# Performance work log

Hardware: AMD Instinct MI355X
Metric: run time of the kernel (lower is better)

Reference implementation:

```python
import math
import jax, jax.numpy as jnp
import numpy as np

FACTOR = 5
N_HEADS = 8


def setup_inputs() -> dict:
    key = jax.random.key(0)
    ks = jax.random.split(key, 9)
    B, S, D = 4, 8192, 512
    s = 0.02
    x = jax.random.normal(ks[0], (B, S, D), jnp.float32)
    Wq = jax.random.normal(ks[1], (D, D), jnp.float32) * s
    bq = jax.random.normal(ks[2], (D,), jnp.float32) * s
    Wk = jax.random.normal(ks[3], (D, D), jnp.float32) * s
    bk = jax.random.normal(ks[4], (D,), jnp.float32) * s
    Wv = jax.random.normal(ks[5], (D, D), jnp.float32) * s
    bv = jax.random.normal(ks[6], (D,), jnp.float32) * s
    Wo = jax.random.normal(ks[7], (D, D), jnp.float32) * s
    bo = jax.random.normal(ks[8], (D,), jnp.float32) * s
    return {"x": x, "Wq": Wq, "bq": bq, "Wk": Wk, "bk": bk,
            "Wv": Wv, "bv": bv, "Wo": Wo, "bo": bo}


def reference(x, Wq, bq, Wk, bk, Wv, bv, Wo, bo):
    B, S, D = x.shape
    H = N_HEADS
    hd = D // H
    scale = hd ** -0.5

    def proj(W, b):
        # [B,S,D] -> [B,H,S,hd]
        return (x @ W + b).reshape(B, S, H, hd).transpose(0, 2, 1, 3)

    q = proj(Wq, bq)
    k = proj(Wk, bk)
    v = proj(Wv, bv)

    # number of "active" queries: O(log S)
    sampled = max(1, min(S, int(FACTOR * math.log(S + 1))))

    sparsity = jnp.sum(q * q, axis=-1)                    # [B,H,S]
    top_idx = jax.lax.top_k(sparsity, sampled)[1]         # [B,H,u]

    sel_q = jnp.take_along_axis(q, top_idx[..., None], axis=2)  # [B,H,u,hd]
    scores = jnp.einsum('bhud,bhsd->bhus', sel_q, k) * scale     # [B,H,u,S]
    attn = jax.nn.softmax(scores, axis=-1)
    sel_ctx = jnp.einsum('bhus,bhsd->bhud', attn, v)             # [B,H,u,hd]

    # default context = mean of values; overwrite rows of selected queries
    ctx = jnp.broadcast_to(v.mean(axis=2, keepdims=True), (B, H, S, hd))
    bi = jnp.arange(B)[:, None, None]
    hi = jnp.arange(H)[None, :, None]
    ctx = ctx.at[bi, hi, top_idx].set(sel_ctx)                   # scatter [B,H,S,hd]

    ctx = ctx.transpose(0, 2, 1, 3).reshape(B, S, D)
    return ctx @ Wo + bo
```

## Files before the change

### kernel.cpp

```cpp
#include <hip/hip_runtime.h>
#include <hip/hip_fp16.h>
#include <math.h>

#define B_ 4
#define S_ 8192
#define D_ 512
#define H_ 8
#define U_ 45
#define NCHUNK 16

typedef unsigned short ushortT;
typedef __attribute__((ext_vector_type(8))) _Float16 half8;
typedef __attribute__((ext_vector_type(4))) float f32x4;

__device__ __forceinline__ ushortT f2h(float f) {
    return __half_as_ushort(__float2half(f));
}
__device__ __forceinline__ float h2f(ushortT u) {
    return __half2float(__ushort_as_half(u));
}

__device__ __forceinline__ void gload_lds16(const ushortT* g, ushortT* l) {
    __builtin_amdgcn_global_load_lds(
        (const __attribute__((address_space(1))) void*)g,
        (__attribute__((address_space(3))) void*)l,
        16, 0, 0);
}

__global__ __launch_bounds__(256) void prep_kernel(
    const float* __restrict__ X, ushortT* __restrict__ Xf,
    const float* __restrict__ Wq, const float* __restrict__ Wk,
    const float* __restrict__ Wv,
    ushortT* __restrict__ WqT, ushortT* __restrict__ WkT,
    ushortT* __restrict__ WvT,
    float* __restrict__ vsum, float* __restrict__ outbase)
{
    __shared__ float t[32][33];
    const int bx = blockIdx.x;
    if (bx < 8192) {
        if (bx == 0) {
            float4 z = {0.f, 0.f, 0.f, 0.f};
            *(float4*)&vsum[threadIdx.x * 8]        = z;
            *(float4*)&vsum[threadIdx.x * 8 + 4]    = z;
            *(float4*)&outbase[threadIdx.x * 8]     = z;
            *(float4*)&outbase[threadIdx.x * 8 + 4] = z;
        }
        size_t i = ((size_t)bx * 256 + threadIdx.x) * 8;
        float4 a = *(const float4*)(X + i);
        float4 b = *(const float4*)(X + i + 4);
        *(ushort4*)(Xf + i)     = make_ushort4(f2h(a.x), f2h(a.y), f2h(a.z), f2h(a.w));
        *(ushort4*)(Xf + i + 4) = make_ushort4(f2h(b.x), f2h(b.y), f2h(b.z), f2h(b.w));
    } else {
        const int idx = bx - 8192;
        const int z = idx >> 8, rem = idx & 255;
        const int r0 = (rem >> 4) * 32, c0 = (rem & 15) * 32;
        const float* W = (z == 0) ? Wq : (z == 1) ? Wk : Wv;
        ushortT* O = (z == 0) ? WqT : (z == 1) ? WkT : WvT;
        const int tx = threadIdx.x & 31, ty4 = (threadIdx.x >> 5) * 4;
#pragma unroll
        for (int i = 0; i < 4; ++i)
            t[ty4 + i][tx] = W[(size_t)(r0 + ty4 + i) * 512 + c0 + tx];
        __syncthreads();
#pragma unroll
        for (int i = 0; i < 4; ++i)
            O[(size_t)(c0 + ty4 + i) * 512 + r0 + tx] = f2h(t[tx][ty4 + i]);
    }
}

__global__ __launch_bounds__(512, 2) void qkv_mfma(
    const ushortT* __restrict__ Xf,
    const ushortT* __restrict__ WqT, const ushortT* __restrict__ WkT,
    const ushortT* __restrict__ WvT,
    const float* __restrict__ bq, const float* __restrict__ bk,
    const float* __restrict__ bv,
    ushortT* __restrict__ Qbuf, ushortT* __restrict__ Kbuf,
    ushortT* __restrict__ VT,
    float* __restrict__ sparsity, float* __restrict__ vsum)
{
    __shared__ ushortT lds[3 * 128 * 64];

    const int tid  = threadIdx.x;
    const int w    = tid >> 6, lane = tid & 63;
    const int quad = lane >> 4, c16 = lane & 15;
    const bool fusedQK = (blockIdx.y < 4);
    const int stream = w >> 2;
    const int aw   = fusedQK ? ((w >> 1) & 1) : (w >> 1);
    const int bw   = w & 1;
    const int m0   = blockIdx.x * 128;
    const int n0   = fusedQK ? (blockIdx.y * 128) : ((blockIdx.y - 4) * 256);

    const int srowL = lane >> 3;
    const int slc   = (((lane & 7) - (srowL & 7)) & 7) * 8;
    const int rrot  = c16 & 7;

    const ushortT* Brd = fusedQK ? (lds + 8192 + stream * 8192) : (lds + 16384);
    const int awBase = aw * 64;
    const int bwBase = bw * 64;

    f32x4 acc[4][4];
#pragma unroll
    for (int i = 0; i < 4; ++i)
#pragma unroll
        for (int j = 0; j < 4; ++j) acc[i][j] = (f32x4){0.f, 0.f, 0.f, 0.f};

    for (int k0 = 0; k0 < 512; k0 += 64) {
        __syncthreads();
        if (fusedQK) {
#pragma unroll
            for (int c = 0; c < 2; ++c) {
                const int R  = c * 64 + w * 8 + srowL;
                const int lb = c * 4096 + w * 512;
                gload_lds16(Xf  + (size_t)(m0 + R) * 512 + k0 + slc, lds + lb);
                gload_lds16(WqT + (size_t)(n0 + R) * 512 + k0 + slc, lds + 8192 + lb);
                gload_lds16(WkT + (size_t)(n0 + R) * 512 + k0 + slc, lds + 16384 + lb);
            }
        } else {
#pragma unroll
            for (int c = 0; c < 4; ++c) {
                const int R = c * 64 + w * 8 + srowL;
                gload_lds16(WvT + (size_t)(n0 + R) * 512 + k0 + slc,
                            lds + c * 4096 + w * 512);
            }
#pragma unroll
            for (int c = 0; c < 2; ++c) {
                const int R = c * 64 + w * 8 + srowL;
                gload_lds16(Xf + (size_t)(m0 + R) * 512 + k0 + slc,
                            lds + 16384 + c * 4096 + w * 512);
            }
        }
        __syncthreads();
#pragma unroll
        for (int kk = 0; kk < 2; ++kk) {
            const int phk = (((kk * 4 + quad) + rrot) & 7) * 8;
            half8 af[4], bf[4];
#pragma unroll
            for (int i = 0; i < 4; ++i) {
                af[i] = *(const half8*)&lds[(awBase + i * 16 + c16) * 64 + phk];
                bf[i] = *(const half8*)&Brd[(bwBase + i * 16 + c16) * 64 + phk];
            }
#pragma unroll
            for (int i = 0; i < 4; ++i)
#pragma unroll
                for (int j = 0; j < 4; ++j)
                    acc[i][j] = __builtin_amdgcn_mfma_f32_16x16x32_f16(af[i], bf[j], acc[i][j], 0, 0, 0);
        }
    }

    const int b = m0 >> 13;
    if (fusedQK && stream == 0) {
        const int head = (n0 + bw * 64) >> 6;
        float bb[4];
#pragma unroll
        for (int j = 0; j < 4; ++j) bb[j] = bq[n0 + bw * 64 + j * 16 + c16];
        ushortT* qbase = Qbuf + ((size_t)(b * 8 + head) * 8192) * 64;
#pragma unroll
        for (int i = 0; i < 4; ++i)
#pragma unroll
            for (int r = 0; r < 4; ++r) {
                const int s = (m0 & 8191) + awBase + i * 16 + quad * 4 + r;
                float p = 0.f;
#pragma unroll
                for (int j = 0; j < 4; ++j) {
                    float v = acc[i][j][r] + bb[j];
                    qbase[(size_t)s * 64 + j * 16 + c16] = f2h(v);
                    p = fmaf(v, v, p);
                }
                p += __shfl_xor(p, 1);
                p += __shfl_xor(p, 2);
                p += __shfl_xor(p, 4);
                p += __shfl_xor(p, 8);
                if (c16 == 0)
                    sparsity[((size_t)b * H_ + head) * S_ + s] = p;
            }
    } else if (fusedQK) {
        const int head = (n0 + bw * 64) >> 6;
        float bb[4];
#pragma unroll
        for (int j = 0; j < 4; ++j) bb[j] = bk[n0 + bw * 64 + j * 16 + c16];
        ushortT* kbase = Kbuf + ((size_t)(b * 8 + head) * 8192) * 64;
#pragma unroll
        for (int i = 0; i < 4; ++i)
#pragma unroll
            for (int r = 0; r < 4; ++r) {
                const int s = (m0 & 8191) + awBase + i * 16 + quad * 4 + r;
#pragma unroll
                for (int j = 0; j < 4; ++j)
                    kbase[(size_t)s * 64 + j * 16 + c16] = f2h(acc[i][j][r] + bb[j]);
            }
    } else {
        const int sbase = (m0 & 8191) + bwBase;
#pragma unroll
        for (int i = 0; i < 4; ++i)
#pragma unroll
            for (int r = 0; r < 4; ++r) {
                const int dcol = n0 + awBase + i * 16 + quad * 4 + r;
                const int head = dcol >> 6, dd = dcol & 63;
                const float biasv = bv[dcol];
                ushortT* vrow = VT + ((size_t)(b * 8 + head) * 64 + dd) * 8192;
                float vsa = 0.f;
#pragma unroll
                for (int j = 0; j < 4; ++j) {
                    float v = acc[i][j][r] + biasv;
                    vrow[sbase + j * 16 + c16] = f2h(v);
                    vsa += v;
                }
                vsa += __shfl_xor(vsa, 1);
                vsa += __shfl_xor(vsa, 2);
                vsa += __shfl_xor(vsa, 4);
                vsa += __shfl_xor(vsa, 8);
                if (c16 == 0) atomicAdd(&vsum[b * 512 + dcol], vsa);
            }
    }
}

__global__ __launch_bounds__(256) void topk_kernel(
    const float* __restrict__ sparsity, int* __restrict__ topidx,
    const float* __restrict__ vsum, const float* __restrict__ Wo,
    const float* __restrict__ bo, float* __restrict__ outbase)
{
    __shared__ unsigned vals[S_];
    __shared__ unsigned hist[8][256];
    __shared__ int ssum[256];
    __shared__ unsigned prefix_s;
    __shared__ int need_s;
    __shared__ int cnt_gt_s, cnt_eq_s;
    __shared__ int eqidx[64];
    const int tid = threadIdx.x;

    if (blockIdx.x >= 32) {
        const int idx = blockIdx.x - 32;
        const int b = idx >> 3, ks = (idx & 7) >> 1, dh = idx & 1;
        const int d = dh * 256 + tid;
        float acc = (ks == 0) ? bo[d] : 0.f;
        const int r0 = ks * 128;
        for (int r = r0; r < r0 + 128; ++r) {
            float mv = vsum[b * 512 + r] * (1.0f / S_);
            acc = fmaf(mv, Wo[(size_t)r * 512 + d], acc);
        }
        atomicAdd(&outbase[b * 512 + d], acc);
        return;
    }

    const int bh = blockIdx.x;
    const unsigned* sp = (const unsigned*)(sparsity + (size_t)bh * S_);
    for (int i = tid; i < S_; i += 256) vals[i] = sp[i];

    unsigned prefix = 0;
    int need = U_;
    const int rep = tid & 7;
    for (int level = 0; level < 4; ++level) {
        const int shift = 24 - level * 8;
#pragma unroll
        for (int r = 0; r < 8; ++r) hist[r][tid] = 0;
        __syncthreads();
        const unsigned pmask = (level == 0) ? 0u : (0xFFFFFFFFu << (shift + 8));
        for (int i = tid; i < S_; i += 256) {
            unsigned v = vals[i];
            if ((v & pmask) == prefix)
                atomicAdd(&hist[rep][(v >> shift) & 255], 1u);
        }
        __syncthreads();
        int bs = 0;
#pragma unroll
        for (int r = 0; r < 8; ++r) bs += (int)hist[r][tid];
        ssum[tid] = bs;
        __syncthreads();
        for (int off = 1; off < 256; off <<= 1) {
            int add = (tid + off < 256) ? ssum[tid + off] : 0;
            __syncthreads();
            ssum[tid] += add;
            __syncthreads();
        }
        int snext = (tid == 255) ? 0 : ssum[tid + 1];
        if (ssum[tid] >= need && snext < need) {
            prefix_s = prefix | ((unsigned)tid << shift);
            need_s = need - snext;
        }
        __syncthreads();
        prefix = prefix_s;
        need = need_s;
        __syncthreads();
    }
    const unsigned T = prefix;
    if (tid == 0) { cnt_gt_s = 0; cnt_eq_s = 0; }
    __syncthreads();
    for (int i = tid; i < S_; i += 256) {
        unsigned v = vals[i];
        if (v > T) {
            int p = atomicAdd(&cnt_gt_s, 1);
            topidx[bh * U_ + p] = i;
        } else if (v == T) {
            int p = atomicAdd(&cnt_eq_s, 1);
            if (p < 64) eqidx[p] = i;
        }
    }
    __syncthreads();
    if (tid == 0) {
        int rem = U_ - cnt_gt_s;
        int n = cnt_eq_s < 64 ? cnt_eq_s : 64;
        for (int a = 0; a < rem; ++a) {
            int best = 1 << 30, bj = 0;
            for (int j = 0; j < n; ++j)
                if (eqidx[j] < best) { best = eqidx[j]; bj = j; }
            topidx[bh * U_ + cnt_gt_s + a] = best;
            eqidx[bj] = 1 << 30;
        }
    }
}

__global__ __launch_bounds__(256, 2) void attn_mfma(
    const ushortT* __restrict__ Qbuf, const ushortT* __restrict__ Kbuf,
    const ushortT* __restrict__ VT, const int* __restrict__ topidx,
    float* __restrict__ pl, float* __restrict__ pacc)
{
    __shared__ float sc[48 * 132];
    __shared__ ushortT Qb[48 * 72];

    const int tid = threadIdx.x;
    const int w = tid >> 6, lane = tid & 63;
    const int quad = lane >> 4, c16 = lane & 15;
    const int bh = blockIdx.y;
    const int s_base = blockIdx.x * 512;

    for (int i = tid; i < 48 * 64; i += 256) {
        int q = i >> 6, d = i & 63;
        float v = 0.f;
        if (q < U_) {
            int s = topidx[bh * U_ + q];
            v = h2f(Qbuf[((size_t)bh * 8192 + s) * 64 + d]) * 0.125f;
        }
        Qb[q * 72 + d] = f2h(v);
    }

    f32x4 O[3];
#pragma unroll
    for (int mt = 0; mt < 3; ++mt) O[mt] = (f32x4){0.f, 0.f, 0.f, 0.f};
    float lacc[12];
#pragma unroll
    for (int qi = 0; qi < 12; ++qi) lacc[qi] = 0.f;

    __syncthreads();

    half8 qa[3][2];
#pragma unroll
    for (int mt = 0; mt < 3; ++mt)
#pragma unroll
        for (int kk = 0; kk < 2; ++kk)
            qa[mt][kk] = *(const half8*)&Qb[(mt * 16 + c16) * 72 + kk * 32 + quad * 8];

    const ushortT* kb  = Kbuf + (size_t)bh * 8192 * 64;
    const ushortT* vtb = VT + ((size_t)bh * 64 + w * 16 + c16) * 8192;

    for (int ci = 0; ci < 4; ++ci) {
        const int s0 = s_base + ci * 128;

        half8 kf[2][2];
#pragma unroll
        for (int nt2 = 0; nt2 < 2; ++nt2)
#pragma unroll
            for (int kk = 0; kk < 2; ++kk)
                kf[nt2][kk] = *(const half8*)&kb[
                    (size_t)(s0 + w * 32 + nt2 * 16 + c16) * 64 + kk * 32 + quad * 8];
        f32x4 sacc[3][2];
#pragma unroll
        for (int mt = 0; mt < 3; ++mt)
#pragma unroll
            for (int nt2 = 0; nt2 < 2; ++nt2) {
                sacc[mt][nt2] = (f32x4){0.f, 0.f, 0.f, 0.f};
#pragma unroll
                for (int kk = 0; kk < 2; ++kk)
                    sacc[mt][nt2] = __builtin_amdgcn_mfma_f32_16x16x32_f16(
                        qa[mt][kk], kf[nt2][kk], sacc[mt][nt2], 0, 0, 0);
            }
#pragma unroll
        for (int mt = 0; mt < 3; ++mt)
#pragma unroll
            for (int nt2 = 0; nt2 < 2; ++nt2)
#pragma unroll
                for (int r = 0; r < 4; ++r)
                    sc[(mt * 16 + quad * 4 + r) * 132 + w * 32 + nt2 * 16 + c16] =
                        sacc[mt][nt2][r];
        __syncthreads();

        half8 vb[4];
#pragma unroll
        for (int kk = 0; kk < 4; ++kk)
            vb[kk] = *(const half8*)&vtb[s0 + kk * 32 + quad * 8];

#pragma unroll
        for (int qi = 0; qi < 12; ++qi) {
            const int q = w * 12 + qi;
            float x0 = sc[q * 132 + lane];
            float x1 = sc[q * 132 + 64 + lane];
            ushortT u0 = f2h(__expf(x0));
            ushortT u1 = f2h(__expf(x1));
            lacc[qi] += h2f(u0) + h2f(u1);
            ushortT* pr = (ushortT*)&sc[q * 132];
            pr[lane] = u0;
            pr[lane + 64] = u1;
        }
        __syncthreads();

#pragma unroll
        for (int mt = 0; mt < 3; ++mt)
#pragma unroll
            for (int kk = 0; kk < 4; ++kk) {
                half8 pa = *(const half8*)((const ushortT*)sc +
                    (size_t)(mt * 16 + c16) * 264 + kk * 32 + quad * 8);
                O[mt] = __builtin_amdgcn_mfma_f32_16x16x32_f16(pa, vb[kk], O[mt], 0, 0, 0);
            }
        __syncthreads();
    }

#pragma unroll
    for (int mt = 0; mt < 3; ++mt)
#pragma unroll
        for (int r = 0; r < 4; ++r) {
            const int q = mt * 16 + quad * 4 + r;
            if (q < U_)
                pacc[(((size_t)bh * NCHUNK + blockIdx.x) * U_ + q) * 64 + w * 16 + c16] =
                    O[mt][r];
        }
#pragma unroll
    for (int qi = 0; qi < 12; ++qi) {
        const int q = w * 12 + qi;
        float ssum = lacc[qi];
#pragma unroll
        for (int off = 1; off < 64; off <<= 1) ssum += __shfl_xor(ssum, off);
        if (lane == 0 && q < U_)
            pl[((size_t)bh * NCHUNK + blockIdx.x) * U_ + q] = ssum;
    }
}

__global__ __launch_bounds__(256) void fill_kernel(
    const float* __restrict__ outbase, float* __restrict__ out)
{
    size_t gid = (size_t)blockIdx.x * 256 + threadIdx.x;
    size_t e0 = gid * 4;
    int b = (int)(e0 >> 22);
    int col = (int)(e0 & 511);
    float4 v = *(const float4*)&outbase[b * 512 + col];
    *(float4*)&out[e0] = v;
}

__global__ __launch_bounds__(512) void corr_out_kernel(
    const float* __restrict__ pl, const float* __restrict__ pacc,
    const float* __restrict__ vsum, const float* __restrict__ Wo,
    const int* __restrict__ topidx, float* __restrict__ out)
{
    __shared__ float corrS[64];
    const int q = blockIdx.x, bh = blockIdx.y;
    const int b = bh >> 3, h = bh & 7, tid = threadIdx.x;
    if (tid < 64) {
        float L = 0.f, a = 0.f;
        for (int c = 0; c < NCHUNK; ++c) {
            L += pl[((size_t)bh * NCHUNK + c) * U_ + q];
            a += pacc[(((size_t)bh * NCHUNK + c) * U_ + q) * 64 + tid];
        }
        corrS[tid] = a / L - vsum[b * 512 + h * 64 + tid] * (1.0f / S_);
    }
    __syncthreads();
    const int s = topidx[bh * U_ + q];
    const int d = tid;
    float delta = 0.f;
#pragma unroll
    for (int r = 0; r < 64; ++r)
        delta = fmaf(corrS[r], Wo[(size_t)(h * 64 + r) * 512 + d], delta);
    atomicAdd(&out[((size_t)b * S_ + s) * 512 + d], delta);
}

extern "C" void kernel_launch(void* const* d_in, const int* in_sizes, int n_in,
                              void* d_out, int out_size, void* d_ws, size_t ws_size,
                              hipStream_t stream)
{
    const float* X  = (const float*)d_in[0];
    const float* Wq = (const float*)d_in[1];
    const float* bq = (const float*)d_in[2];
    const float* Wk = (const float*)d_in[3];
    const float* bk = (const float*)d_in[4];
    const float* Wv = (const float*)d_in[5];
    const float* bv = (const float*)d_in[6];
    const float* Wo = (const float*)d_in[7];
    const float* bo = (const float*)d_in[8];
    float* out = (float*)d_out;

    char* ws = (char*)d_ws;
    size_t off = 0;
    auto alloc = [&](size_t bytes) {
        void* p = ws + off;
        off = (off + bytes + 255) & ~(size_t)255;
        return p;
    };
    ushortT* Xf   = (ushortT*)alloc((size_t)B_ * S_ * D_ * 2);
    ushortT* Qbuf = (ushortT*)alloc((size_t)B_ * S_ * D_ * 2);
    ushortT* Kbuf = (ushortT*)alloc((size_t)B_ * S_ * D_ * 2);
    ushortT* VT   = (ushortT*)alloc((size_t)B_ * S_ * D_ * 2);
    ushortT* WqT  = (ushortT*)alloc((size_t)D_ * D_ * 2);
    ushortT* WkT  = (ushortT*)alloc((size_t)D_ * D_ * 2);
    ushortT* WvT  = (ushortT*)alloc((size_t)D_ * D_ * 2);
    float* sparsity = (float*)alloc((size_t)B_ * H_ * S_ * 4);
    int*   topidx   = (int*)alloc((size_t)B_ * H_ * U_ * 4);
    float* pl       = (float*)alloc((size_t)B_ * H_ * NCHUNK * U_ * 4);
    float* pacc     = (float*)alloc((size_t)B_ * H_ * NCHUNK * U_ * 64 * 4);
    float* vsum     = (float*)alloc((size_t)B_ * 512 * 4);
    float* outbase  = (float*)alloc((size_t)B_ * 512 * 4);

    prep_kernel<<<8960, 256, 0, stream>>>(X, Xf, Wq, Wk, Wv, WqT, WkT, WvT,
                                          vsum, outbase);
    qkv_mfma<<<dim3(256, 6), 512, 0, stream>>>(Xf, WqT, WkT, WvT,
                                               bq, bk, bv, Qbuf, Kbuf, VT,
                                               sparsity, vsum);
    topk_kernel<<<64, 256, 0, stream>>>(sparsity, topidx, vsum, Wo, bo, outbase);
    attn_mfma<<<dim3(NCHUNK, B_ * H_), 256, 0, stream>>>(Qbuf, Kbuf, VT, topidx,
                                                         pl, pacc);
    fill_kernel<<<(B_ * S_ * D_ / 4 + 255) / 256, 256, 0, stream>>>(outbase, out);
    corr_out_kernel<<<dim3(U_, B_ * H_), 512, 0, stream>>>(pl, pacc, vsum, Wo,
                                                           topidx, out);
}
```

Before: 279.6 us.

## Recompute selected Q rows in topk kernel; fold output fill into attention launch

The QKV GEMM no longer writes the full Q tensor to global memory and only emits sparsity norms. The topk kernel now gathers the selected X rows and recomputes their Q projections with MFMA, writing a small scaled selQ buffer that attention reads directly. The broadcast fill of the output is merged into the attention launch as extra blocks, which removes one kernel launch. This cuts a large Q write and its later gather, in exchange for extra serial work in the 32-block topk kernel, and the Q used for scoring now differs slightly from the Q used for sparsity.

```diff
diff --git a/kernel.cpp b/kernel.cpp
--- a/kernel.cpp
+++ b/kernel.cpp
@@ -73,8 +73,7 @@
     const ushortT* __restrict__ WvT,
     const float* __restrict__ bq, const float* __restrict__ bk,
     const float* __restrict__ bv,
-    ushortT* __restrict__ Qbuf, ushortT* __restrict__ Kbuf,
-    ushortT* __restrict__ VT,
+    ushortT* __restrict__ Kbuf, ushortT* __restrict__ VT,
     float* __restrict__ sparsity, float* __restrict__ vsum)
 {
     __shared__ ushortT lds[3 * 128 * 64];
@@ -152,7 +151,6 @@
         float bb[4];
 #pragma unroll
         for (int j = 0; j < 4; ++j) bb[j] = bq[n0 + bw * 64 + j * 16 + c16];
-        ushortT* qbase = Qbuf + ((size_t)(b * 8 + head) * 8192) * 64;
 #pragma unroll
         for (int i = 0; i < 4; ++i)
 #pragma unroll
@@ -162,7 +160,6 @@
 #pragma unroll
                 for (int j = 0; j < 4; ++j) {
                     float v = acc[i][j][r] + bb[j];
-                    qbase[(size_t)s * 64 + j * 16 + c16] = f2h(v);
                     p = fmaf(v, v, p);
                 }
                 p += __shfl_xor(p, 1);
@@ -216,15 +213,19 @@
 __global__ __launch_bounds__(256) void topk_kernel(
     const float* __restrict__ sparsity, int* __restrict__ topidx,
     const float* __restrict__ vsum, const float* __restrict__ Wo,
-    const float* __restrict__ bo, float* __restrict__ outbase)
+    const float* __restrict__ bo, float* __restrict__ outbase,
+    const ushortT* __restrict__ Xf, const ushortT* __restrict__ WqT,
+    const float* __restrict__ bq, ushortT* __restrict__ selQ)
 {
-    __shared__ unsigned vals[S_];
-    __shared__ unsigned hist[8][256];
-    __shared__ int ssum[256];
+    __shared__ __align__(16) char smem[49920];
+    unsigned* vals        = (unsigned*)smem;
+    unsigned (*hist)[256] = (unsigned (*)[256])(smem + 32768);
+    int* ssum             = (int*)(smem + 40960);
+    int* eqidx            = (int*)(smem + 41984);
+    ushortT* selX         = (ushortT*)smem;
     __shared__ unsigned prefix_s;
     __shared__ int need_s;
     __shared__ int cnt_gt_s, cnt_eq_s;
-    __shared__ int eqidx[64];
     const int tid = threadIdx.x;
 
     if (blockIdx.x >= 32) {
@@ -306,32 +307,73 @@
             eqidx[bj] = 1 << 30;
         }
     }
+    __syncthreads();
+
+    const int b = bh >> 3, h = bh & 7;
+    for (int i = tid; i < 48 * 64; i += 256) {
+        const int row = i >> 6, ch = i & 63;
+        half8 v;
+#pragma unroll
+        for (int z = 0; z < 8; ++z) v[z] = (_Float16)0.0f;
+        if (row < U_) {
+            const int s = topidx[bh * U_ + row];
+            v = *(const half8*)&Xf[((size_t)b * 8192 + s) * 512 + ch * 8];
+        }
+        *(half8*)&selX[row * 520 + ch * 8] = v;
+    }
+    __syncthreads();
+
+    const int w = tid >> 6, lane = tid & 63;
+    const int quad = lane >> 4, c16 = lane & 15;
+    f32x4 qacc[3];
+#pragma unroll
+    for (int mt = 0; mt < 3; ++mt) qacc[mt] = (f32x4){0.f, 0.f, 0.f, 0.f};
+    const ushortT* brow = WqT + (size_t)(h * 64 + w * 16 + c16) * 512;
+    for (int k0 = 0; k0 < 512; k0 += 32) {
+        half8 bf = *(const half8*)&brow[k0 + quad * 8];
+#pragma unroll
+        for (int mt = 0; mt < 3; ++mt) {
+            half8 af = *(const half8*)&selX[(mt * 16 + c16) * 520 + k0 + quad * 8];
+            qacc[mt] = __builtin_amdgcn_mfma_f32_16x16x32_f16(af, bf, qacc[mt], 0, 0, 0);
+        }
+    }
+    const float bb = bq[h * 64 + w * 16 + c16];
+    ushortT* oq = selQ + (size_t)bh * 48 * 64 + (w * 16 + c16);
+#pragma unroll
+    for (int mt = 0; mt < 3; ++mt)
+#pragma unroll
+        for (int r = 0; r < 4; ++r) {
+            const int m = mt * 16 + quad * 4 + r;
+            float v = (m < U_) ? (qacc[mt][r] + bb) * 0.125f : 0.f;
+            oq[(size_t)m * 64] = f2h(v);
+        }
 }
 
 __global__ __launch_bounds__(256, 2) void attn_mfma(
-    const ushortT* __restrict__ Qbuf, const ushortT* __restrict__ Kbuf,
-    const ushortT* __restrict__ VT, const int* __restrict__ topidx,
-    float* __restrict__ pl, float* __restrict__ pacc)
+    const ushortT* __restrict__ selQ, const ushortT* __restrict__ Kbuf,
+    const ushortT* __restrict__ VT,
+    float* __restrict__ pl, float* __restrict__ pacc,
+    const float* __restrict__ outbase, float* __restrict__ out)
 {
     __shared__ float sc[48 * 132];
-    __shared__ ushortT Qb[48 * 72];
 
     const int tid = threadIdx.x;
+
+    if (blockIdx.x >= NCHUNK) {
+        const int unit = (blockIdx.x - NCHUNK) * 32 + blockIdx.y;
+        size_t e0 = ((size_t)unit * 256 + tid) * 4;
+        int b = (int)(e0 >> 22);
+        int col = (int)(e0 & 511);
+        float4 v = *(const float4*)&outbase[b * 512 + col];
+        *(float4*)&out[e0] = v;
+        return;
+    }
+
     const int w = tid >> 6, lane = tid & 63;
     const int quad = lane >> 4, c16 = lane & 15;
     const int bh = blockIdx.y;
     const int s_base = blockIdx.x * 512;
 
-    for (int i = tid; i < 48 * 64; i += 256) {
-        int q = i >> 6, d = i & 63;
-        float v = 0.f;
-        if (q < U_) {
-            int s = topidx[bh * U_ + q];
-            v = h2f(Qbuf[((size_t)bh * 8192 + s) * 64 + d]) * 0.125f;
-        }
-        Qb[q * 72 + d] = f2h(v);
-    }
-
     f32x4 O[3];
 #pragma unroll
     for (int mt = 0; mt < 3; ++mt) O[mt] = (f32x4){0.f, 0.f, 0.f, 0.f};
@@ -339,14 +381,13 @@
 #pragma unroll
     for (int qi = 0; qi < 12; ++qi) lacc[qi] = 0.f;
 
-    __syncthreads();
-
+    const ushortT* sq = selQ + (size_t)bh * 48 * 64;
     half8 qa[3][2];
 #pragma unroll
     for (int mt = 0; mt < 3; ++mt)
 #pragma unroll
         for (int kk = 0; kk < 2; ++kk)
-            qa[mt][kk] = *(const half8*)&Qb[(mt * 16 + c16) * 72 + kk * 32 + quad * 8];
+            qa[mt][kk] = *(const half8*)&sq[(mt * 16 + c16) * 64 + kk * 32 + quad * 8];
 
     const ushortT* kb  = Kbuf + (size_t)bh * 8192 * 64;
     const ushortT* vtb = VT + ((size_t)bh * 64 + w * 16 + c16) * 8192;
@@ -430,17 +471,6 @@
         if (lane == 0 && q < U_)
             pl[((size_t)bh * NCHUNK + blockIdx.x) * U_ + q] = ssum;
     }
-}
-
-__global__ __launch_bounds__(256) void fill_kernel(
-    const float* __restrict__ outbase, float* __restrict__ out)
-{
-    size_t gid = (size_t)blockIdx.x * 256 + threadIdx.x;
-    size_t e0 = gid * 4;
-    int b = (int)(e0 >> 22);
-    int col = (int)(e0 & 511);
-    float4 v = *(const float4*)&outbase[b * 512 + col];
-    *(float4*)&out[e0] = v;
 }
 
 __global__ __launch_bounds__(512) void corr_out_kernel(
@@ -492,12 +522,12 @@
         return p;
     };
     ushortT* Xf   = (ushortT*)alloc((size_t)B_ * S_ * D_ * 2);
-    ushortT* Qbuf = (ushortT*)alloc((size_t)B_ * S_ * D_ * 2);
     ushortT* Kbuf = (ushortT*)alloc((size_t)B_ * S_ * D_ * 2);
     ushortT* VT   = (ushortT*)alloc((size_t)B_ * S_ * D_ * 2);
     ushortT* WqT  = (ushortT*)alloc((size_t)D_ * D_ * 2);
     ushortT* WkT  = (ushortT*)alloc((size_t)D_ * D_ * 2);
     ushortT* WvT  = (ushortT*)alloc((size_t)D_ * D_ * 2);
+    ushortT* selQ = (ushortT*)alloc((size_t)B_ * H_ * 48 * 64 * 2);
     float* sparsity = (float*)alloc((size_t)B_ * H_ * S_ * 4);
     int*   topidx   = (int*)alloc((size_t)B_ * H_ * U_ * 4);
     float* pl       = (float*)alloc((size_t)B_ * H_ * NCHUNK * U_ * 4);
@@ -508,12 +538,12 @@
     prep_kernel<<<8960, 256, 0, stream>>>(X, Xf, Wq, Wk, Wv, WqT, WkT, WvT,
                                           vsum, outbase);
     qkv_mfma<<<dim3(256, 6), 512, 0, stream>>>(Xf, WqT, WkT, WvT,
-                                               bq, bk, bv, Qbuf, Kbuf, VT,
+                                               bq, bk, bv, Kbuf, VT,
                                                sparsity, vsum);
-    topk_kernel<<<64, 256, 0, stream>>>(sparsity, topidx, vsum, Wo, bo, outbase);
-    attn_mfma<<<dim3(NCHUNK, B_ * H_), 256, 0, stream>>>(Qbuf, Kbuf, VT, topidx,
-                                                         pl, pacc);
-    fill_kernel<<<(B_ * S_ * D_ / 4 + 255) / 256, 256, 0, stream>>>(outbase, out);
+    topk_kernel<<<64, 256, 0, stream>>>(sparsity, topidx, vsum, Wo, bo, outbase,
+                                        Xf, WqT, bq, selQ);
+    attn_mfma<<<dim3(NCHUNK + 512, B_ * H_), 256, 0, stream>>>(
+        selQ, Kbuf, VT, pl, pacc, outbase, out);
     corr_out_kernel<<<dim3(U_, B_ * H_), 512, 0, stream>>>(pl, pacc, vsum, Wo,
                                                            topidx, out);
 }
```

Measured after the change: 285.3 us. +2.0%, slower.
